# Kernel optimization log

Measured on AMD Instinct MI355X. Metric: run time of the kernel, lower is better.

## Reference

```python
import jax, jax.numpy as jnp
import numpy as np

B, T, TRAIN = 4, 2048, 1536
D, H, L, FF, V = 512, 8, 12, 2048, 100
DH = D // H
ROPE_BASE = 100000.0


def layer_norm(x, g, b, eps=1e-5):
    mu = jnp.mean(x, axis=-1, keepdims=True)
    var = jnp.mean(jnp.square(x - mu), axis=-1, keepdims=True)
    return (x - mu) * jax.lax.rsqrt(var + eps) * g + b


def rope_cos_sin(t, dh):
    inv_freq = 1.0 / (ROPE_BASE ** (jnp.arange(0, dh, 2, dtype=jnp.float32) / dh))  # (dh/2,)
    ang = jnp.arange(t, dtype=jnp.float32)[:, None] * inv_freq[None, :]  # (T, dh/2)
    return jnp.cos(ang), jnp.sin(ang)


def apply_rope_interleaved(x, cos, sin):
    # x: (B, T, H, DH); interleaved pairs (x0,x1),(x2,x3),...
    x1, x2 = x[..., 0::2], x[..., 1::2]
    c, s = cos[None, :, None, :], sin[None, :, None, :]
    r1 = x1 * c - x2 * s
    r2 = x1 * s + x2 * c
    return jnp.stack([r1, r2], axis=-1).reshape(x.shape)


def setup_inputs() -> dict:
    key = jax.random.key(0)
    ks = jax.random.split(key, 20)
    sc = 0.02
    inp = {
        'R': jax.random.normal(ks[0], (B, T, D), jnp.float32),
        'y_train': jax.random.randint(ks[1], (B, TRAIN), 0, V),
        'emb': jax.random.normal(ks[2], (V, D), jnp.float32) * sc,
        'Wqkv': jax.random.normal(ks[3], (L, D, 3 * D), jnp.float32) * sc,
        'bqkv': jnp.zeros((L, 3 * D), jnp.float32),
        'Wo': jax.random.normal(ks[4], (L, D, D), jnp.float32) * sc,
        'bo': jnp.zeros((L, D), jnp.float32),
        'ln1_g': jnp.ones((L, D), jnp.float32),
        'ln1_b': jnp.zeros((L, D), jnp.float32),
        'ln2_g': jnp.ones((L, D), jnp.float32),
        'ln2_b': jnp.zeros((L, D), jnp.float32),
        'W1': jax.random.normal(ks[5], (L, D, FF), jnp.float32) * sc,
        'b1': jnp.zeros((L, FF), jnp.float32),
        'W2': jax.random.normal(ks[6], (L, FF, D), jnp.float32) * sc,
        'b2': jnp.zeros((L, D), jnp.float32),
        'pW1': jax.random.normal(ks[7], (D, 2 * D), jnp.float32) * sc,
        'pb1': jnp.zeros((2 * D,), jnp.float32),
        'pW2': jax.random.normal(ks[8], (2 * D, V), jnp.float32) * sc,
        'pb2': jnp.zeros((V,), jnp.float32),
    }
    return inp


def icl_forward(R, y_train, emb, Wqkv, bqkv, Wo, bo, ln1_g, ln1_b, ln2_g, ln2_b, W1, b1, W2, b2, pW1, pb1, pW2, pb2):
    b, t, d = R.shape
    train = y_train.shape[1]
    # label embedding: train rows get emb[y], test rows get zeros
    y_emb = jnp.concatenate([emb[y_train], jnp.zeros((b, t - train, d), R.dtype)], axis=1)
    rep = R + y_emb
    # ICL mask: column j visible iff j < train or j == i
    idx = jnp.arange(t)
    allowed = (idx[None, :] < train) | (idx[:, None] == idx[None, :])
    mask = jnp.where(allowed, 0.0, -jnp.inf).astype(R.dtype)  # (T, T)
    cos, sin = rope_cos_sin(t, DH)
    scale = 1.0 / jnp.sqrt(jnp.asarray(DH, R.dtype))

    def block(x, p):
        wqkv, bq, wo, bob, g1, be1, g2, be2, w1, bb1, w2, bb2 = p
        h = layer_norm(x, g1, be1)
        qkv = h @ wqkv + bq  # (B,T,3D)
        q, k, v = jnp.split(qkv, 3, axis=-1)
        q = q.reshape(b, t, H, DH)
        k = k.reshape(b, t, H, DH)
        v = v.reshape(b, t, H, DH)
        q = apply_rope_interleaved(q, cos, sin)
        k = apply_rope_interleaved(k, cos, sin)
        scores = jnp.einsum('bthd,bshd->bhts', q, k) * scale + mask
        attn = jax.nn.softmax(scores, axis=-1)
        o = jnp.einsum('bhts,bshd->bthd', attn, v).reshape(b, t, d)
        x = x + o @ wo + bob
        h2 = layer_norm(x, g2, be2)
        x = x + jax.nn.gelu(h2 @ w1 + bb1) @ w2 + bb2
        return x, None

    rep, _ = jax.lax.scan(block, rep, (Wqkv, bqkv, Wo, bo, ln1_g, ln1_b, ln2_g, ln2_b, W1, b1, W2, b2))
    test = rep[:, train:, :]
    logits = jax.nn.gelu(test @ pW1 + pb1) @ pW2 + pb2  # (B, test, V)
    return logits


def reference(R, y_train, emb, Wqkv, bqkv, Wo, bo, ln1_g, ln1_b, ln2_g, ln2_b, W1, b1, W2, b2, pW1, pb1, pW2, pb2):
    return icl_forward(R, y_train, emb, Wqkv, bqkv, Wo, bo, ln1_g, ln1_b, ln2_g, ln2_b, W1, b1, W2, b2, pW1, pb1, pW2, pb2)
```

## Files before the change

### kernel.cpp

```cpp
#include <hip/hip_runtime.h>
#include <hip/hip_bf16.h>

#define BB 4
#define TT 2048
#define TRAIN 1536
#define DD 512
#define HH 8
#define LL 12
#define FFD 2048
#define VV 100
#define DH 64
#define NT (BB*TT)
#define NTEST (BB*(TT-TRAIN))

typedef __bf16 bf16x8 __attribute__((ext_vector_type(8)));
typedef float  f32x4  __attribute__((ext_vector_type(4)));
typedef unsigned int u32x4 __attribute__((ext_vector_type(4)));

#define GLDS16(g, l) __builtin_amdgcn_global_load_lds( \
    (const __attribute__((address_space(1))) void*)(g), \
    (__attribute__((address_space(3))) void*)(l), 16, 0, 0)

__global__ __launch_bounds__(256) void emb_add(const float* __restrict__ R,
                                               const int* __restrict__ y,
                                               const float* __restrict__ emb,
                                               float* __restrict__ rep) {
    int idx = blockIdx.x * 256 + threadIdx.x;
    int d = idx & 511;
    int n = idx >> 9;
    int t = n & (TT - 1);
    int b = n >> 11;
    float val = R[idx];
    if (t < TRAIN) {
        int tok = y[b * TRAIN + t];
        val += emb[(size_t)tok * DD + d];
    }
    rep[idx] = val;
}

__global__ __launch_bounds__(256) void ln_wave(const float* __restrict__ x,
                                               const float* __restrict__ g,
                                               const float* __restrict__ bta,
                                               __bf16* __restrict__ out) {
    int row = blockIdx.x * 4 + (threadIdx.x >> 6);
    int lane = threadIdx.x & 63;
    const float* xr = x + (size_t)row * DD + lane * 8;
    float4 a = *(const float4*)xr;
    float4 c = *(const float4*)(xr + 4);
    float s  = a.x + a.y + a.z + a.w + c.x + c.y + c.z + c.w;
    float sq = a.x*a.x + a.y*a.y + a.z*a.z + a.w*a.w + c.x*c.x + c.y*c.y + c.z*c.z + c.w*c.w;
#pragma unroll
    for (int off = 1; off < 64; off <<= 1) {
        s  += __shfl_xor(s, off);
        sq += __shfl_xor(sq, off);
    }
    float mu  = s * (1.0f / DD);
    float var = sq * (1.0f / DD) - mu * mu;
    float inv = rsqrtf(var + 1e-5f);
    const float* gp = g + lane * 8;
    const float* bp = bta + lane * 8;
    float4 g0 = *(const float4*)gp, g1 = *(const float4*)(gp + 4);
    float4 b0 = *(const float4*)bp, b1 = *(const float4*)(bp + 4);
    __bf16 o8[8];
    o8[0] = (__bf16)((a.x - mu) * inv * g0.x + b0.x);
    o8[1] = (__bf16)((a.y - mu) * inv * g0.y + b0.y);
    o8[2] = (__bf16)((a.z - mu) * inv * g0.z + b0.z);
    o8[3] = (__bf16)((a.w - mu) * inv * g0.w + b0.w);
    o8[4] = (__bf16)((c.x - mu) * inv * g1.x + b1.x);
    o8[5] = (__bf16)((c.y - mu) * inv * g1.y + b1.y);
    o8[6] = (__bf16)((c.z - mu) * inv * g1.z + b1.z);
    o8[7] = (__bf16)((c.w - mu) * inv * g1.w + b1.w);
    *(uint4*)(out + (size_t)row * DD + lane * 8) = *(uint4*)o8;
}

__global__ __launch_bounds__(256) void rope_tab(float* __restrict__ ctab, float* __restrict__ stab) {
    int idx = blockIdx.x * 256 + threadIdx.x;
    int p = idx & 31, t = idx >> 5;
    double freq = exp(-((double)(2 * p) / 64.0) * log(100000.0));
    double ang = (double)t * freq;
    ctab[idx] = (float)cos(ang);
    stab[idx] = (float)sin(ang);
}

__global__ __launch_bounds__(256) void rope_vt(const __bf16* __restrict__ qkv,
                                               const float* __restrict__ ctab,
                                               const float* __restrict__ stab,
                                               __bf16* __restrict__ qo,
                                               __bf16* __restrict__ ko,
                                               __bf16* __restrict__ vt) {
    int bh = blockIdx.y; int b = bh >> 3, h = bh & 7;
    int t0 = blockIdx.x * 64;
    __shared__ __bf16 tile[64][72];
    int tid = threadIdx.x;
    {
        int r = tid >> 2, cg = (tid & 3) * 16;
        const __bf16* src = qkv + (size_t)(b * TT + t0 + r) * (3 * DD) + 2 * DD + h * DH + cg;
        *(uint4*)&tile[r][cg]     = *(const uint4*)&src[0];
        *(uint4*)&tile[r][cg + 8] = *(const uint4*)&src[8];
    }
#pragma unroll
    for (int c = 0; c < 8; ++c) {
        int pidx = c * 256 + tid;
        int tl = pidx >> 5, p = pidx & 31;
        int t = t0 + tl;
        const __bf16* base = qkv + (size_t)(b * TT + t) * (3 * DD) + h * DH;
        float co = ctab[t * 32 + p], si = stab[t * 32 + p];
        float x1 = (float)base[2 * p],       x2 = (float)base[2 * p + 1];
        float k1 = (float)base[DD + 2 * p], k2 = (float)base[DD + 2 * p + 1];
        size_t ob = ((size_t)bh * TT + t) * DH;
        qo[ob + 2 * p]     = (__bf16)(x1 * co - x2 * si);
        qo[ob + 2 * p + 1] = (__bf16)(x1 * si + x2 * co);
        ko[ob + 2 * p]     = (__bf16)(k1 * co - k2 * si);
        ko[ob + 2 * p + 1] = (__bf16)(k1 * si + k2 * co);
    }
    __syncthreads();
    {
        int dh = tid >> 2, tg = (tid & 3) * 16;
        __bf16 outv[16];
#pragma unroll
        for (int j = 0; j < 16; ++j) outv[j] = tile[tg + j][dh];
        __bf16* dst = vt + ((size_t)bh * DH + dh) * TT + t0 + tg;
        *(uint4*)&dst[0] = *(uint4*)&outv[0];
        *(uint4*)&dst[8] = *(uint4*)&outv[8];
    }
}

#define NCH (TRAIN/128)

__global__ __launch_bounds__(256, 2) void attn_mfma(const __bf16* __restrict__ q,
                                                    const __bf16* __restrict__ k,
                                                    const __bf16* __restrict__ vt,
                                                    __bf16* __restrict__ obuf) {
    __shared__ __align__(16) __bf16 Kb[2][128 * 64];
    __shared__ __align__(16) __bf16 Vb[64 * 128];
    __shared__ float sself[128];

    const int tid = threadIdx.x;
    const int lin = blockIdx.x;
    const int xcd = lin & 7, sblk = lin >> 3;
    const int bh = xcd * 4 + (sblk & 3);
    const int t0q = (sblk >> 2) * 128;
    const int b = bh >> 3, hh = bh & 7;
    const size_t kbase = (size_t)bh * TT * DH;
    const int w = tid >> 6;
    const int lane = tid & 63;
    const int l16 = lane & 15;
    const int quad = lane >> 4;
    const int x7 = l16 & 7;

    bf16x8 qa[2][2];
#pragma unroll
    for (int mi = 0; mi < 2; ++mi)
#pragma unroll
        for (int ks = 0; ks < 2; ++ks) {
            const __bf16* qg = q + kbase + (size_t)(t0q + w * 32 + mi * 16 + l16) * DH + ks * 32 + quad * 8;
            uint4 u = *(const uint4*)qg;
            const __bf16* pb = (const __bf16*)&u;
            bf16x8 vq;
#pragma unroll
            for (int j = 0; j < 8; ++j) vq[j] = (__bf16)((float)pb[j] * 0.125f);
            qa[mi][ks] = vq;
        }

    const int krl = lane >> 3, ksl = lane & 7;
    const int vrl = lane >> 4, vsl = lane & 15;

    f32x4 oa[2][4] = {};
    float lsum[2] = {0.f, 0.f};

    {
        const __bf16* g = k + kbase;
#pragma unroll
        for (int c = 0; c < 4; ++c) {
            int rb = w * 4 + c;
            GLDS16(g + (size_t)(rb * 8 + krl) * DH + ((ksl ^ krl) * 8), &Kb[0][rb * 512]);
        }
    }

    for (int ci = 0; ci < NCH; ++ci) {
        __syncthreads();
#pragma unroll
        for (int c = 0; c < 4; ++c) {
            int rb = w * 4 + c;
            int dh = rb * 4 + vrl;
            GLDS16(vt + kbase + (size_t)dh * TT + ci * 128 + ((vsl ^ (dh & 7)) * 8), &Vb[rb * 512]);
        }

        const __bf16* kc = Kb[ci & 1];
        f32x4 acc[2][8] = {};
        __builtin_amdgcn_s_setprio(1);
#pragma unroll
        for (int ks = 0; ks < 2; ++ks) {
            bf16x8 kf[8];
#pragma unroll
            for (int ni = 0; ni < 8; ++ni)
                kf[ni] = *(const bf16x8*)&kc[(ni * 16 + l16) * 64 + (((ks * 4 + quad) ^ x7) * 8)];
#pragma unroll
            for (int ni = 0; ni < 8; ++ni) {
                acc[0][ni] = __builtin_amdgcn_mfma_f32_16x16x32_bf16(kf[ni], qa[0][ks], acc[0][ni], 0, 0, 0);
                acc[1][ni] = __builtin_amdgcn_mfma_f32_16x16x32_bf16(kf[ni], qa[1][ks], acc[1][ni], 0, 0, 0);
            }
        }
        __builtin_amdgcn_s_setprio(0);

        u32x4 pa[2][4];
#pragma unroll
        for (int mi = 0; mi < 2; ++mi) {
            unsigned int pk[8][2];
            float rs = 0.f;
#pragma unroll
            for (int ni = 0; ni < 8; ++ni) {
                float p0 = __expf(acc[mi][ni][0]);
                float p1 = __expf(acc[mi][ni][1]);
                float p2 = __expf(acc[mi][ni][2]);
                float p3 = __expf(acc[mi][ni][3]);
                rs += (p0 + p1) + (p2 + p3);
                asm("v_cvt_pk_bf16_f32 %0, %1, %2" : "=v"(pk[ni][0]) : "v"(p0), "v"(p1));
                asm("v_cvt_pk_bf16_f32 %0, %1, %2" : "=v"(pk[ni][1]) : "v"(p2), "v"(p3));
            }
            rs += __shfl_xor(rs, 16);
            rs += __shfl_xor(rs, 32);
            lsum[mi] += rs;
#pragma unroll
            for (int ks = 0; ks < 4; ++ks)
#pragma unroll
                for (int rr = 0; rr < 2; ++rr) {
                    unsigned int A = pk[2 * ks][rr], Bv = pk[2 * ks + 1][rr];
                    asm("v_permlane32_swap_b32 %0, %1" : "+v"(A), "+v"(Bv));
                    asm("v_permlane16_swap_b32 %0, %1" : "+v"(A), "+v"(Bv));
                    pa[mi][ks][rr]     = A;
                    pa[mi][ks][rr + 2] = Bv;
                }
        }

        __syncthreads();
        if (ci + 1 < NCH) {
            const __bf16* g = k + kbase + (size_t)((ci + 1) * 128) * DH;
            __bf16* dst = Kb[(ci + 1) & 1];
#pragma unroll
            for (int c = 0; c < 4; ++c) {
                int rb = w * 4 + c;
                GLDS16(g + (size_t)(rb * 8 + krl) * DH + ((ksl ^ krl) * 8), dst + rb * 512);
            }
        }

        __builtin_amdgcn_s_setprio(1);
#pragma unroll
        for (int ks = 0; ks < 4; ++ks) {
            bf16x8 vf[4];
#pragma unroll
            for (int ni = 0; ni < 4; ++ni)
                vf[ni] = *(const bf16x8*)&Vb[(ni * 16 + l16) * 128 + (((ks * 4 + quad) ^ x7) * 8)];
            bf16x8 pa0, pa1;
            { u32x4 t = pa[0][ks]; __builtin_memcpy(&pa0, &t, 16); }
            { u32x4 t = pa[1][ks]; __builtin_memcpy(&pa1, &t, 16); }
#pragma unroll
            for (int ni = 0; ni < 4; ++ni) {
                oa[0][ni] = __builtin_amdgcn_mfma_f32_16x16x32_bf16(pa0, vf[ni], oa[0][ni], 0, 0, 0);
                oa[1][ni] = __builtin_amdgcn_mfma_f32_16x16x32_bf16(pa1, vf[ni], oa[1][ni], 0, 0, 0);
            }
        }
        __builtin_amdgcn_s_setprio(0);
    }

    float lr[2][4];
#pragma unroll
    for (int mi = 0; mi < 2; ++mi)
#pragma unroll
        for (int r = 0; r < 4; ++r)
            lr[mi][r] = __shfl(lsum[mi], quad * 4 + r);

    if (t0q >= TRAIN) {
        __syncthreads();
        {
            int dh = tid >> 2, cg = (tid & 3) * 32;
            const __bf16* vg = vt + kbase + (size_t)dh * TT + t0q + cg;
#pragma unroll
            for (int u = 0; u < 4; ++u)
                *(uint4*)&Vb[dh * 128 + cg + u * 8] = *(const uint4*)&vg[u * 8];
            int row = tid >> 1, hf = tid & 1;
            const __bf16* qp = q + kbase + (size_t)(t0q + row) * DH + hf * 32;
            const __bf16* kp = k + kbase + (size_t)(t0q + row) * DH + hf * 32;
            float dacc = 0.f;
#pragma unroll
            for (int u = 0; u < 4; ++u) {
                uint4 uq = *(const uint4*)&qp[u * 8];
                uint4 uk = *(const uint4*)&kp[u * 8];
                const __bf16* pq = (const __bf16*)&uq;
                const __bf16* pk2 = (const __bf16*)&uk;
#pragma unroll
                for (int j = 0; j < 8; ++j) dacc += (float)pq[j] * (float)pk2[j];
            }
            dacc += __shfl_xor(dacc, 1);
            sself[row] = dacc * 0.125f;
        }
        __syncthreads();
#pragma unroll
        for (int mi = 0; mi < 2; ++mi)
#pragma unroll
            for (int r = 0; r < 4; ++r) {
                int qr = w * 32 + mi * 16 + quad * 4 + r;
                float pp = __expf(sself[qr]);
                lr[mi][r] += pp;
#pragma unroll
                for (int ni = 0; ni < 4; ++ni)
                    oa[mi][ni][r] += pp * (float)Vb[(ni * 16 + l16) * 128 + qr];
            }
    }

#pragma unroll
    for (int mi = 0; mi < 2; ++mi)
#pragma unroll
        for (int r = 0; r < 4; ++r) {
            float inv = 1.f / lr[mi][r];
            int trow = t0q + w * 32 + mi * 16 + quad * 4 + r;
            __bf16* op = obuf + ((size_t)(b * TT) + trow) * DD + hh * 64;
#pragma unroll
            for (int ni = 0; ni < 4; ++ni)
                op[ni * 16 + l16] = (__bf16)(oa[mi][ni][r] * inv);
        }
}

__global__ __launch_bounds__(256) void transpose_pad(const float* __restrict__ src,
                                                     __bf16* __restrict__ dst,
                                                     int K, int N) {
    __shared__ __bf16 t[32][33];
    int n0 = blockIdx.x * 32, k0 = blockIdx.y * 32;
    int tx = threadIdx.x & 31, ty = threadIdx.x >> 5;
#pragma unroll
    for (int i = 0; i < 4; ++i) {
        int nn = n0 + tx;
        t[ty + i * 8][tx] = (nn < N) ? (__bf16)src[(size_t)(k0 + ty + i * 8) * N + nn] : (__bf16)0.f;
    }
    __syncthreads();
#pragma unroll
    for (int i = 0; i < 4; ++i) {
        dst[(size_t)(n0 + ty + i * 8) * K + k0 + tx] = t[tx][ty + i * 8];
    }
}

__global__ __launch_bounds__(256) void transpose_all(const float* __restrict__ s0,
                                                     const float* __restrict__ s1,
                                                     const float* __restrict__ s2,
                                                     const float* __restrict__ s3,
                                                     __bf16* __restrict__ d0, __bf16* __restrict__ d1,
                                                     __bf16* __restrict__ d2, __bf16* __restrict__ d3) {
    int i = blockIdx.x;
    const float* src; __bf16* dst; int K, N, tx, ty;
    if (i < 768)       { src = s0; dst = d0; K = 512;  N = 1536; int j = i;        tx = j % 48; ty = j / 48; }
    else if (i < 1024) { src = s1; dst = d1; K = 512;  N = 512;  int j = i - 768;  tx = j % 16; ty = j / 16; }
    else if (i < 2048) { src = s2; dst = d2; K = 512;  N = 2048; int j = i - 1024; tx = j % 64; ty = j / 64; }
    else               { src = s3; dst = d3; K = 2048; N = 512;  int j = i - 2048; tx = j % 16; ty = j / 16; }
    __shared__ __bf16 t[32][33];
    int n0 = tx * 32, k0 = ty * 32;
    int lx = threadIdx.x & 31, ly = threadIdx.x >> 5;
#pragma unroll
    for (int c = 0; c < 4; ++c)
        t[ly + c * 8][lx] = (__bf16)src[(size_t)(k0 + ly + c * 8) * N + n0 + lx];
    __syncthreads();
#pragma unroll
    for (int c = 0; c < 4; ++c)
        dst[(size_t)(n0 + ly + c * 8) * K + k0 + lx] = t[lx][ly + c * 8];
}

template <int EP, int TN>
__global__ __launch_bounds__(256) void gemm_bt(const __bf16* __restrict__ A,
                                               const __bf16* __restrict__ Bt,
                                               const float* __restrict__ bias,
                                               float* __restrict__ resid,
                                               __bf16* __restrict__ Cout,
                                               int M, int N, int K) {
    constexpr int NI = TN / 32;
    __shared__ __align__(16) __bf16 As[2][128 * 32];
    __shared__ __align__(16) __bf16 Bs[2][TN * 32];
    const int tid = threadIdx.x;
    const int gx = gridDim.x;
    const int linb = blockIdx.x + gx * blockIdx.y;
    const int xs = gx >> 3;
    const int xcd = linb & 7, sb = linb >> 3;
    const int bx = xcd * xs + (sb % xs);
    const int by = sb / xs;
    const int m0 = bx * 128;
    const int n0 = by * TN;
    const int lane = tid & 63;
    const int w = tid >> 6;
    const int wm = (w >> 1) * 64, wn = (w & 1) * (TN / 2);
    const int lrow = lane & 15;
    const int kq = (lane >> 4) * 8;

    f32x4 acc[4][NI] = {};

    const int srA = w * 32 + (lane >> 2);
    const int srB = w * (TN / 4) + (lane >> 2);
    const int scol = (lane & 3) * 8;
    const __bf16* gA = A  + (size_t)(m0 + srA) * K + scol;
    const __bf16* gB = Bt + (size_t)(n0 + srB) * K + scol;
    __bf16* lA0 = &As[0][(w * 32) * 32];
    __bf16* lA0b = lA0 + 16 * 32;
    __bf16* lA1 = &As[1][(w * 32) * 32];
    __bf16* lA1b = lA1 + 16 * 32;
    __bf16* lB0 = &Bs[0][(w * (TN / 4)) * 32];
    __bf16* lB1 = &Bs[1][(w * (TN / 4)) * 32];

    const int nk = K >> 6;
    for (int kt = 0; kt < nk; ++kt) {
        const int k0 = kt << 6;
        GLDS16(gA + k0,            lA0);
        GLDS16(gA + 16 * K + k0,   lA0b);
        GLDS16(gA + k0 + 32,       lA1);
        GLDS16(gA + 16 * K + k0 + 32, lA1b);
        GLDS16(gB + k0,            lB0);
        GLDS16(gB + k0 + 32,       lB1);
        if constexpr (TN == 128) {
            GLDS16(gB + 16 * K + k0,      lB0 + 16 * 32);
            GLDS16(gB + 16 * K + k0 + 32, lB1 + 16 * 32);
        }
        __syncthreads();
#pragma unroll
        for (int ps = 0; ps < 2; ++ps) {
            bf16x8 afr[4], bfr[NI];
#pragma unroll
            for (int i = 0; i < 4; ++i)
                afr[i] = *(const bf16x8*)&As[ps][(wm + i * 16 + lrow) * 32 + kq];
#pragma unroll
            for (int i = 0; i < NI; ++i)
                bfr[i] = *(const bf16x8*)&Bs[ps][(wn + i * 16 + lrow) * 32 + kq];
#pragma unroll
            for (int mi = 0; mi < 4; ++mi)
#pragma unroll
                for (int ni = 0; ni < NI; ++ni)
                    acc[mi][ni] = __builtin_amdgcn_mfma_f32_16x16x32_bf16(afr[mi], bfr[ni], acc[mi][ni], 0, 0, 0);
        }
        __syncthreads();
    }

    const int crow = (lane >> 4) * 4;
    const int ccol = lane & 15;
#pragma unroll
    for (int mi = 0; mi < 4; ++mi) {
#pragma unroll
        for (int ni = 0; ni < NI; ++ni) {
            int gn = n0 + wn + ni * 16 + ccol;
            float bv = bias[gn];
#pragma unroll
            for (int r = 0; r < 4; ++r) {
                int gm = m0 + wm + mi * 16 + crow + r;
                float vvv = acc[mi][ni][r] + bv;
                if constexpr (EP == 1) {
                    float x = vvv;
                    vvv = x / (1.f + __expf(-1.5957691216f * (x + 0.044715f * x * x * x)));
                }
                if constexpr (EP == 2) {
                    resid[(size_t)gm * N + gn] += vvv;
                } else if constexpr (EP == 4) {
                    if (gn < VV) resid[(size_t)gm * VV + gn] = vvv;
                } else {
                    Cout[(size_t)gm * N + gn] = (__bf16)vvv;
                }
            }
        }
    }
}

__global__ __launch_bounds__(256) void cast_test(const float* __restrict__ rep, __bf16* __restrict__ testb) {
    int idx = blockIdx.x * 256 + threadIdx.x;
    int d = idx & 511;
    int i = idx >> 9;
    int ttk = i & 511;
    int b = i >> 9;
    testb[idx] = (__bf16)rep[(size_t)(b * TT + TRAIN + ttk) * DD + d];
}

__global__ void pad_bias(const float* __restrict__ pb2, float* __restrict__ pb2p) {
    int t = threadIdx.x;
    if (t < 128) pb2p[t] = (t < VV) ? pb2[t] : 0.f;
}

extern "C" void kernel_launch(void* const* d_in, const int* in_sizes, int n_in,
                              void* d_out, int out_size, void* d_ws, size_t ws_size,
                              hipStream_t stream) {
    const float* R    = (const float*)d_in[0];
    const int*   y    = (const int*)d_in[1];
    const float* emb  = (const float*)d_in[2];
    const float* Wqkv = (const float*)d_in[3];
    const float* bqkv = (const float*)d_in[4];
    const float* Wo   = (const float*)d_in[5];
    const float* bo   = (const float*)d_in[6];
    const float* ln1g = (const float*)d_in[7];
    const float* ln1b = (const float*)d_in[8];
    const float* ln2g = (const float*)d_in[9];
    const float* ln2b = (const float*)d_in[10];
    const float* W1   = (const float*)d_in[11];
    const float* b1   = (const float*)d_in[12];
    const float* W2   = (const float*)d_in[13];
    const float* b2   = (const float*)d_in[14];
    const float* pW1  = (const float*)d_in[15];
    const float* pb1  = (const float*)d_in[16];
    const float* pW2  = (const float*)d_in[17];
    const float* pb2  = (const float*)d_in[18];

    char* p = (char*)d_ws;
    float* rep    = (float*)p;  p += (size_t)NT * DD * 4;
    __bf16* hbuf  = (__bf16*)p; p += (size_t)NT * DD * 2;
    __bf16* qkv   = (__bf16*)p;
    __bf16* ffb   = qkv;        p += (size_t)NT * FFD * 2;
    __bf16* qb    = (__bf16*)p; p += (size_t)NT * DD * 2;
    __bf16* kb    = (__bf16*)p; p += (size_t)NT * DD * 2;
    __bf16* vtb   = (__bf16*)p; p += (size_t)NT * DD * 2;
    __bf16* obuf  = (__bf16*)p; p += (size_t)NT * DD * 2;
    __bf16* wqkvT = (__bf16*)p; p += (size_t)1536 * 512 * 2;
    __bf16* woT   = (__bf16*)p; p += (size_t)512 * 512 * 2;
    __bf16* w1T   = (__bf16*)p; p += (size_t)2048 * 512 * 2;
    __bf16* w2T   = (__bf16*)p; p += (size_t)512 * 2048 * 2;
    float* ctab   = (float*)p;  p += (size_t)TT * 32 * 4;
    float* stab   = (float*)p;  p += (size_t)TT * 32 * 4;
    float* pb2p   = (float*)p;  p += 512;
    __bf16* testb = hbuf;
    __bf16* hb    = obuf;

    emb_add<<<NT * DD / 256, 256, 0, stream>>>(R, y, emb, rep);
    rope_tab<<<TT * 32 / 256, 256, 0, stream>>>(ctab, stab);

    for (int l = 0; l < LL; ++l) {
        ln_wave<<<NT / 4, 256, 0, stream>>>(rep, ln1g + l * DD, ln1b + l * DD, hbuf);
        transpose_all<<<3072, 256, 0, stream>>>(Wqkv + (size_t)l * DD * 3 * DD, Wo + (size_t)l * DD * DD,
                                                W1 + (size_t)l * DD * FFD, W2 + (size_t)l * FFD * DD,
                                                wqkvT, woT, w1T, w2T);
        gemm_bt<0, 128><<<dim3(NT / 128, 1536 / 128), 256, 0, stream>>>(hbuf, wqkvT, bqkv + l * 3 * DD, nullptr, qkv, NT, 3 * DD, DD);
        rope_vt<<<dim3(TT / 64, BB * HH), 256, 0, stream>>>(qkv, ctab, stab, qb, kb, vtb);
        attn_mfma<<<dim3(512), 256, 0, stream>>>(qb, kb, vtb, obuf);
        gemm_bt<2, 64><<<dim3(NT / 128, 512 / 64), 256, 0, stream>>>(obuf, woT, bo + l * DD, rep, nullptr, NT, DD, DD);
        ln_wave<<<NT / 4, 256, 0, stream>>>(rep, ln2g + l * DD, ln2b + l * DD, hbuf);
        gemm_bt<1, 128><<<dim3(NT / 128, FFD / 128), 256, 0, stream>>>(hbuf, w1T, b1 + l * FFD, nullptr, ffb, NT, FFD, DD);
        gemm_bt<2, 64><<<dim3(NT / 128, 512 / 64), 256, 0, stream>>>(ffb, w2T, b2 + l * DD, rep, nullptr, NT, DD, FFD);
    }

    cast_test<<<NTEST * DD / 256, 256, 0, stream>>>(rep, testb);
    transpose_pad<<<dim3(1024 / 32, 512 / 32), 256, 0, stream>>>(pW1, w1T, DD, 2 * DD);
    gemm_bt<1, 64><<<dim3(NTEST / 128, 1024 / 64), 256, 0, stream>>>(testb, w1T, pb1, nullptr, hb, NTEST, 2 * DD, DD);
    pad_bias<<<1, 128, 0, stream>>>(pb2, pb2p);
    transpose_pad<<<dim3(128 / 32, 1024 / 32), 256, 0, stream>>>(pW2, w2T, 2 * DD, VV);
    gemm_bt<4, 128><<<dim3(NTEST / 128, 1), 256, 0, stream>>>(hb, w2T, pb2p, (float*)d_out, nullptr, NTEST, 128, 2 * DD);
}
```

Before: 2.298 ms.

## Double-buffer V tiles in attention, vectorize RoPE, fold softmax scale into Q

The attention kernel now double-buffers V in LDS alongside K. The next chunk's K and V are prefetched at the top of each iteration, which removes one __syncthreads per chunk and overlaps V loads with compute. The RoPE kernel is rewritten to use 16-byte vector loads and stores of q/k and float4 cos/sin, and it applies the 1/sqrt(dh) scale to Q there. Q fragments are then loaded directly without per-element rescaling. The cost is double the LDS used for V, which may affect the occupancy of 2 blocks per CU, plus a slight rounding change from scaling before the bf16 cast.

Measured after the change: 2.295 ms. Within noise of the previous version (-0.2%).

```diff
diff --git a/kernel.cpp b/kernel.cpp
--- a/kernel.cpp
+++ b/kernel.cpp
@@ -99,19 +99,32 @@
         *(uint4*)&tile[r][cg + 8] = *(const uint4*)&src[8];
     }
 #pragma unroll
-    for (int c = 0; c < 8; ++c) {
-        int pidx = c * 256 + tid;
-        int tl = pidx >> 5, p = pidx & 31;
+    for (int c = 0; c < 2; ++c) {
+        int lin = c * 256 + tid;
+        int tl = lin >> 3, u = lin & 7;
         int t = t0 + tl;
-        const __bf16* base = qkv + (size_t)(b * TT + t) * (3 * DD) + h * DH;
-        float co = ctab[t * 32 + p], si = stab[t * 32 + p];
-        float x1 = (float)base[2 * p],       x2 = (float)base[2 * p + 1];
-        float k1 = (float)base[DD + 2 * p], k2 = (float)base[DD + 2 * p + 1];
-        size_t ob = ((size_t)bh * TT + t) * DH;
-        qo[ob + 2 * p]     = (__bf16)(x1 * co - x2 * si);
-        qo[ob + 2 * p + 1] = (__bf16)(x1 * si + x2 * co);
-        ko[ob + 2 * p]     = (__bf16)(k1 * co - k2 * si);
-        ko[ob + 2 * p + 1] = (__bf16)(k1 * si + k2 * co);
+        const __bf16* base = qkv + (size_t)(b * TT + t) * (3 * DD) + h * DH + u * 8;
+        uint4 qu = *(const uint4*)base;
+        uint4 ku = *(const uint4*)(base + DD);
+        float4 cv = *(const float4*)(ctab + t * 32 + u * 4);
+        float4 sv = *(const float4*)(stab + t * 32 + u * 4);
+        const __bf16* qp = (const __bf16*)&qu;
+        const __bf16* kp = (const __bf16*)&ku;
+        float cc[4] = {cv.x, cv.y, cv.z, cv.w};
+        float ss[4] = {sv.x, sv.y, sv.z, sv.w};
+        __bf16 oq[8], ok8[8];
+#pragma unroll
+        for (int j = 0; j < 4; ++j) {
+            float x1 = (float)qp[2 * j], x2 = (float)qp[2 * j + 1];
+            float k1 = (float)kp[2 * j], k2 = (float)kp[2 * j + 1];
+            oq[2 * j]     = (__bf16)((x1 * cc[j] - x2 * ss[j]) * 0.125f);
+            oq[2 * j + 1] = (__bf16)((x1 * ss[j] + x2 * cc[j]) * 0.125f);
+            ok8[2 * j]     = (__bf16)(k1 * cc[j] - k2 * ss[j]);
+            ok8[2 * j + 1] = (__bf16)(k1 * ss[j] + k2 * cc[j]);
+        }
+        size_t ob = ((size_t)bh * TT + t) * DH + u * 8;
+        *(uint4*)(qo + ob) = *(uint4*)oq;
+        *(uint4*)(ko + ob) = *(uint4*)ok8;
     }
     __syncthreads();
     {
@@ -132,7 +145,7 @@
                                                     const __bf16* __restrict__ vt,
                                                     __bf16* __restrict__ obuf) {
     __shared__ __align__(16) __bf16 Kb[2][128 * 64];
-    __shared__ __align__(16) __bf16 Vb[64 * 128];
+    __shared__ __align__(16) __bf16 Vb[2][64 * 128];
     __shared__ float sself[128];
 
     const int tid = threadIdx.x;
@@ -154,12 +167,7 @@
 #pragma unroll
         for (int ks = 0; ks < 2; ++ks) {
             const __bf16* qg = q + kbase + (size_t)(t0q + w * 32 + mi * 16 + l16) * DH + ks * 32 + quad * 8;
-            uint4 u = *(const uint4*)qg;
-            const __bf16* pb = (const __bf16*)&u;
-            bf16x8 vq;
-#pragma unroll
-            for (int j = 0; j < 8; ++j) vq[j] = (__bf16)((float)pb[j] * 0.125f);
-            qa[mi][ks] = vq;
+            qa[mi][ks] = *(const bf16x8*)qg;
         }
 
     const int krl = lane >> 3, ksl = lane & 7;
@@ -169,21 +177,28 @@
     float lsum[2] = {0.f, 0.f};
 
     {
-        const __bf16* g = k + kbase;
 #pragma unroll
         for (int c = 0; c < 4; ++c) {
             int rb = w * 4 + c;
-            GLDS16(g + (size_t)(rb * 8 + krl) * DH + ((ksl ^ krl) * 8), &Kb[0][rb * 512]);
+            GLDS16(k + kbase + (size_t)(rb * 8 + krl) * DH + ((ksl ^ krl) * 8), &Kb[0][rb * 512]);
+            int dh = rb * 4 + vrl;
+            GLDS16(vt + kbase + (size_t)dh * TT + ((vsl ^ (dh & 7)) * 8), &Vb[0][rb * 512]);
         }
     }
 
     for (int ci = 0; ci < NCH; ++ci) {
         __syncthreads();
-#pragma unroll
-        for (int c = 0; c < 4; ++c) {
-            int rb = w * 4 + c;
-            int dh = rb * 4 + vrl;
-            GLDS16(vt + kbase + (size_t)dh * TT + ci * 128 + ((vsl ^ (dh & 7)) * 8), &Vb[rb * 512]);
+        if (ci + 1 < NCH) {
+            const __bf16* gk = k + kbase + (size_t)((ci + 1) * 128) * DH;
+            __bf16* dK = Kb[(ci + 1) & 1];
+            __bf16* dV = Vb[(ci + 1) & 1];
+#pragma unroll
+            for (int c = 0; c < 4; ++c) {
+                int rb = w * 4 + c;
+                GLDS16(gk + (size_t)(rb * 8 + krl) * DH + ((ksl ^ krl) * 8), dK + rb * 512);
+                int dh = rb * 4 + vrl;
+                GLDS16(vt + kbase + (size_t)dh * TT + (ci + 1) * 128 + ((vsl ^ (dh & 7)) * 8), dV + rb * 512);
+            }
         }
 
         const __bf16* kc = Kb[ci & 1];
@@ -233,24 +248,14 @@
                 }
         }
 
-        __syncthreads();
-        if (ci + 1 < NCH) {
-            const __bf16* g = k + kbase + (size_t)((ci + 1) * 128) * DH;
-            __bf16* dst = Kb[(ci + 1) & 1];
-#pragma unroll
-            for (int c = 0; c < 4; ++c) {
-                int rb = w * 4 + c;
-                GLDS16(g + (size_t)(rb * 8 + krl) * DH + ((ksl ^ krl) * 8), dst + rb * 512);
-            }
-        }
-
+        const __bf16* vc = Vb[ci & 1];
         __builtin_amdgcn_s_setprio(1);
 #pragma unroll
         for (int ks = 0; ks < 4; ++ks) {
             bf16x8 vf[4];
 #pragma unroll
             for (int ni = 0; ni < 4; ++ni)
-                vf[ni] = *(const bf16x8*)&Vb[(ni * 16 + l16) * 128 + (((ks * 4 + quad) ^ x7) * 8)];
+                vf[ni] = *(const bf16x8*)&vc[(ni * 16 + l16) * 128 + (((ks * 4 + quad) ^ x7) * 8)];
             bf16x8 pa0, pa1;
             { u32x4 t = pa[0][ks]; __builtin_memcpy(&pa0, &t, 16); }
             { u32x4 t = pa[1][ks]; __builtin_memcpy(&pa1, &t, 16); }
@@ -277,7 +282,7 @@
             const __bf16* vg = vt + kbase + (size_t)dh * TT + t0q + cg;
 #pragma unroll
             for (int u = 0; u < 4; ++u)
-                *(uint4*)&Vb[dh * 128 + cg + u * 8] = *(const uint4*)&vg[u * 8];
+                *(uint4*)&Vb[0][dh * 128 + cg + u * 8] = *(const uint4*)&vg[u * 8];
             int row = tid >> 1, hf = tid & 1;
             const __bf16* qp = q + kbase + (size_t)(t0q + row) * DH + hf * 32;
             const __bf16* kp = k + kbase + (size_t)(t0q + row) * DH + hf * 32;
@@ -292,7 +297,7 @@
                 for (int j = 0; j < 8; ++j) dacc += (float)pq[j] * (float)pk2[j];
             }
             dacc += __shfl_xor(dacc, 1);
-            sself[row] = dacc * 0.125f;
+            sself[row] = dacc;
         }
         __syncthreads();
 #pragma unroll
@@ -304,7 +309,7 @@
                 lr[mi][r] += pp;
 #pragma unroll
                 for (int ni = 0; ni < 4; ++ni)
-                    oa[mi][ni][r] += pp * (float)Vb[(ni * 16 + l16) * 128 + qr];
+                    oa[mi][ni][r] += pp * (float)Vb[0][(ni * 16 + l16) * 128 + qr];
             }
     }
 
```
